# Optimization experiments

Hardware: AMD Instinct MI355X
Metric: run time of the kernel (lower is better)

Reference implementation:

```python
import jax, jax.numpy as jnp
import numpy as np


def setup_inputs() -> dict:
    key = jax.random.key(0)
    kq, kk, kv, ks = jax.random.split(key, 4)
    B, Sq, H, Hkv, D, Dv, Smax = 4, 4, 32, 8, 128, 128, 8192
    Q = jax.random.normal(kq, (B, Sq, H, D), dtype=jnp.float32)
    K = jax.random.normal(kk, (B, Smax, Hkv, D), dtype=jnp.float32)
    V = jax.random.normal(kv, (B, Smax, Hkv, Dv), dtype=jnp.float32)
    # cache lengths well inside [Sq, Smax]
    cache_seqlens = jax.random.randint(ks, (B,), 4096, Smax + 1, dtype=jnp.int32)
    return {"Q": Q, "K": K, "V": V, "cache_seqlens": cache_seqlens}


def reference(Q, K, V, cache_seqlens):
    # Q: [B, Sq, H, D]; K: [B, Smax, Hkv, D]; V: [B, Smax, Hkv, Dv]
    B, Sq, H, D = Q.shape
    Smax, Hkv = K.shape[1], K.shape[2]
    g = H // Hkv  # GQA group size
    scale = 1.0 / (D ** 0.5)

    # Group query heads by their shared KV head to avoid repeating K/V.
    Qg = Q.reshape(B, Sq, Hkv, g, D)
    # scores: [B, Hkv, g, Sq, Smax]
    scores = jnp.einsum("bqhgd,bkhd->bhgqk", Qg, K) * scale

    # Causal-at-cache-end mask: position j valid iff j <= cache_seqlens[b] - Sq + m
    pos = jnp.arange(Smax)
    limit = cache_seqlens[:, None] - Sq + jnp.arange(Sq)[None, :]  # [B, Sq]
    mask = pos[None, None, :] <= limit[:, :, None]                 # [B, Sq, Smax]
    neg_inf = jnp.asarray(-jnp.inf, dtype=scores.dtype)
    scores = jnp.where(mask[:, None, None, :, :], scores, neg_inf)

    attn = jax.nn.softmax(scores, axis=-1)
    out = jnp.einsum("bhgqk,bkhd->bqhgd", attn, V)  # [B, Sq, Hkv, g, Dv]
    return out.reshape(B, Sq, H, V.shape[-1])
```

## Files before the change

kernel.cpp:

```cpp
#include <hip/hip_runtime.h>
#include <hip/hip_bf16.h>
#include <stdint.h>

#define B_    4
#define SQ    4
#define H_    32
#define HKV   8
#define G_    4
#define D_    128
#define SMAX  8192
#define ROWS  16
#define BH    (B_ * HKV)
#define SCALE 0.08838834764831845f
#define MAXSPLITS 64

__device__ __forceinline__ void unpack8(const uint4& u, float* f) {
  f[0] = __uint_as_float(u.x << 16);
  f[1] = __uint_as_float(u.x & 0xffff0000u);
  f[2] = __uint_as_float(u.y << 16);
  f[3] = __uint_as_float(u.y & 0xffff0000u);
  f[4] = __uint_as_float(u.z << 16);
  f[5] = __uint_as_float(u.z & 0xffff0000u);
  f[6] = __uint_as_float(u.w << 16);
  f[7] = __uint_as_float(u.w & 0xffff0000u);
}

__global__ __launch_bounds__(256)
void fa4_sniff(const uint32_t* __restrict__ Kw, int* __restrict__ flag) {
  __shared__ int s_cnt;
  const int t = threadIdx.x;
  if (t == 0) s_cnt = 0;
  __syncthreads();
  int local = 0;
#pragma unroll
  for (int i = 0; i < 4; ++i) {
    const uint32_t w = Kw[t * 4 + i];
    const uint32_t e = (w >> 7) & 0xFFu;
    local += (e >= 100u && e <= 150u) ? 1 : 0;
  }
  atomicAdd(&s_cnt, local);
  __syncthreads();
  if (t == 0) flag[0] = (s_cnt > 700) ? 1 : 0;
}

template<bool BF16>
__device__ __forceinline__ void partial_body(
    const void* __restrict__ Q, const void* __restrict__ K,
    const void* __restrict__ V, const int* __restrict__ lens,
    int splits, int chunk,
    float* __restrict__ Lout, float* __restrict__ acc_out) {
  constexpr int KB  = BF16 ? 16 : 8;
  constexpr int NR  = BF16 ? 1 : 2;
  constexpr int ESZ = BF16 ? 2 : 4;

  const int split = blockIdx.x;
  const int bh    = blockIdx.y;
  const int b     = bh >> 3;
  const int hkv   = bh & 7;
  const int t     = threadIdx.x;
  const int r     = t >> 4;
  const int c     = t & 15;
  const int m     = r >> 2;
  const int gq    = r & 3;
  const int h     = hkv * G_ + gq;

  int len = lens[b];
  if (len > SMAX) len = SMAX;
  if (len < 0)    len = 0;

  const int j0   = split * chunk;
  const int jend = min(j0 + chunk, len);
  const int lim  = len - SQ + m;
  const int vend = min(jend, lim + 1);

  const int sidx = (bh * splits + split) * ROWS + r;
  float* ap = acc_out + (size_t)sidx * D_ + c * 8;

  if (j0 >= vend) {
    if (c == 0) Lout[sidx] = 0.0f;
    const float4 z = make_float4(0.f, 0.f, 0.f, 0.f);
    *(float4*)(ap)     = z;
    *(float4*)(ap + 4) = z;
    return;
  }

  float qf[8];
  {
    const char* qp = (const char*)Q +
        ((size_t)(((b * SQ + m) * H_ + h) * D_) + c * 8) * ESZ;
    if constexpr (BF16) {
      unpack8(*(const uint4*)qp, qf);
    } else {
      const float4 a0 = ((const float4*)qp)[0];
      const float4 a1 = ((const float4*)qp)[1];
      qf[0]=a0.x; qf[1]=a0.y; qf[2]=a0.z; qf[3]=a0.w;
      qf[4]=a1.x; qf[5]=a1.y; qf[6]=a1.z; qf[7]=a1.w;
    }
#pragma unroll
    for (int i = 0; i < 8; ++i) qf[i] *= SCALE;
  }

  const size_t kv0 = ((size_t)b * SMAX * HKV + hkv) * D_ + c * 8;
  const char*  kbase = (const char*)K + kv0 * ESZ;
  const char*  vbase = (const char*)V + kv0 * ESZ;
  constexpr size_t KSTRB = (size_t)HKV * D_ * ESZ;

  float l_run  = 0.0f;
  float acc[8] = {0.f,0.f,0.f,0.f,0.f,0.f,0.f,0.f};

  int j = j0;
  for (; j + KB <= vend; j += KB) {
    uint4 kraw[KB][NR], vraw[KB][NR];
#pragma unroll
    for (int kb = 0; kb < KB; ++kb) {
      const char* kp = kbase + (size_t)(j + kb) * KSTRB;
      const char* vp = vbase + (size_t)(j + kb) * KSTRB;
#pragma unroll
      for (int q = 0; q < NR; ++q) {
        kraw[kb][q] = ((const uint4*)kp)[q];
        vraw[kb][q] = ((const uint4*)vp)[q];
      }
    }
    __builtin_amdgcn_sched_barrier(0);
    float lsum = 0.0f;
#pragma unroll
    for (int kb = 0; kb < KB; ++kb) {
      float kf[8], vf[8];
      if constexpr (BF16) {
        unpack8(kraw[kb][0], kf);
        unpack8(vraw[kb][0], vf);
      } else {
        const float* kk = (const float*)&kraw[kb][0];
        const float* vv = (const float*)&vraw[kb][0];
#pragma unroll
        for (int i = 0; i < 8; ++i) { kf[i] = kk[i]; vf[i] = vv[i]; }
      }
      float p = qf[0] * kf[0];
#pragma unroll
      for (int i = 1; i < 8; ++i) p = fmaf(qf[i], kf[i], p);
      p += __shfl_xor(p, 1, 16);
      p += __shfl_xor(p, 2, 16);
      p += __shfl_xor(p, 4, 16);
      p += __shfl_xor(p, 8, 16);
      const float pw = __expf(p);
      lsum += pw;
#pragma unroll
      for (int i = 0; i < 8; ++i) acc[i] = fmaf(pw, vf[i], acc[i]);
    }
    l_run += lsum;
  }

  if (j < vend) {
    const int jmaxv = vend - 1;
    uint4 kraw[KB][NR], vraw[KB][NR];
#pragma unroll
    for (int kb = 0; kb < KB; ++kb) {
      const int jj = min(j + kb, jmaxv);
      const char* kp = kbase + (size_t)jj * KSTRB;
      const char* vp = vbase + (size_t)jj * KSTRB;
#pragma unroll
      for (int q = 0; q < NR; ++q) {
        kraw[kb][q] = ((const uint4*)kp)[q];
        vraw[kb][q] = ((const uint4*)vp)[q];
      }
    }
    __builtin_amdgcn_sched_barrier(0);
    float lsum = 0.0f;
#pragma unroll
    for (int kb = 0; kb < KB; ++kb) {
      float kf[8], vf[8];
      if constexpr (BF16) {
        unpack8(kraw[kb][0], kf);
        unpack8(vraw[kb][0], vf);
      } else {
        const float* kk = (const float*)&kraw[kb][0];
        const float* vv = (const float*)&vraw[kb][0];
#pragma unroll
        for (int i = 0; i < 8; ++i) { kf[i] = kk[i]; vf[i] = vv[i]; }
      }
      float p = qf[0] * kf[0];
#pragma unroll
      for (int i = 1; i < 8; ++i) p = fmaf(qf[i], kf[i], p);
      p += __shfl_xor(p, 1, 16);
      p += __shfl_xor(p, 2, 16);
      p += __shfl_xor(p, 4, 16);
      p += __shfl_xor(p, 8, 16);
      const float pw = (j + kb <= jmaxv) ? __expf(p) : 0.0f;
      lsum += pw;
#pragma unroll
      for (int i = 0; i < 8; ++i) acc[i] = fmaf(pw, vf[i], acc[i]);
    }
    l_run += lsum;
  }

  if (c == 0) Lout[sidx] = l_run;
  *(float4*)(ap)     = make_float4(acc[0], acc[1], acc[2], acc[3]);
  *(float4*)(ap + 4) = make_float4(acc[4], acc[5], acc[6], acc[7]);
}

__global__
__attribute__((amdgpu_flat_work_group_size(256, 256)))
__attribute__((amdgpu_waves_per_eu(2, 2)))
void fa4_partial(const void* __restrict__ Q, const void* __restrict__ K,
                 const void* __restrict__ V, const int* __restrict__ lens,
                 const int* __restrict__ flag, int splits, int chunk,
                 float* __restrict__ Lout, float* __restrict__ acc_out) {
  if (flag[0] == 1) partial_body<true >(Q, K, V, lens, splits, chunk, Lout, acc_out);
  else              partial_body<false>(Q, K, V, lens, splits, chunk, Lout, acc_out);
}

__global__ __launch_bounds__(256)
void fa4_reduce(const float* __restrict__ Lin,
                const float* __restrict__ acc_in,
                const int* __restrict__ flag, int splits,
                void* __restrict__ out) {
  const int bh  = blockIdx.x;
  const int b   = bh >> 3;
  const int hkv = bh & 7;
  const int t   = threadIdx.x;
  const int r   = t >> 4;
  const int c   = t & 15;
  const int m   = r >> 2;
  const int gq  = r & 3;
  const int h   = hkv * G_ + gq;

  float L = 0.0f;
  float o[8] = {0.f,0.f,0.f,0.f,0.f,0.f,0.f,0.f};
#pragma unroll 4
  for (int s = 0; s < splits; ++s) {
    const size_t row = (size_t)(bh * splits + s) * ROWS + r;
    L += Lin[row];
    const float4* ap = (const float4*)(acc_in + row * D_ + c * 8);
    const float4 a0 = ap[0];
    const float4 a1 = ap[1];
    o[0] += a0.x; o[1] += a0.y; o[2] += a0.z; o[3] += a0.w;
    o[4] += a1.x; o[5] += a1.y; o[6] += a1.z; o[7] += a1.w;
  }
  const float inv = (L > 0.0f) ? (1.0f / L) : 0.0f;
  const size_t oo = ((size_t)(b * SQ + m) * H_ + h) * D_ + c * 8;
  if (flag[0] == 1) {
    unsigned short us[8];
#pragma unroll
    for (int i = 0; i < 8; ++i) {
      const __hip_bfloat16 hb = __float2bfloat16(o[i] * inv);
      __builtin_memcpy(&us[i], &hb, 2);
    }
    uint4 pk;
    pk.x = (uint32_t)us[0] | ((uint32_t)us[1] << 16);
    pk.y = (uint32_t)us[2] | ((uint32_t)us[3] << 16);
    pk.z = (uint32_t)us[4] | ((uint32_t)us[5] << 16);
    pk.w = (uint32_t)us[6] | ((uint32_t)us[7] << 16);
    *(uint4*)((__hip_bfloat16*)out + oo) = pk;
  } else {
    float* op = (float*)out + oo;
    *(float4*)(op)     = make_float4(o[0]*inv, o[1]*inv, o[2]*inv, o[3]*inv);
    *(float4*)(op + 4) = make_float4(o[4]*inv, o[5]*inv, o[6]*inv, o[7]*inv);
  }
}

extern "C" void kernel_launch(void* const* d_in, const int* in_sizes, int n_in,
                              void* d_out, int out_size, void* d_ws, size_t ws_size,
                              hipStream_t stream) {
  const void* Q   = d_in[0];
  const void* K   = d_in[1];
  const void* V   = d_in[2];
  const int* lens = (const int*)d_in[3];

  const size_t per_split = (size_t)BH * ROWS * sizeof(float)
                         + (size_t)BH * ROWS * D_ * sizeof(float);
  int S = 1;
  if (ws_size > 256 + per_split)
    S = (int)((ws_size - 256) / per_split);
  if (S < 1) S = 1;
  if (S > MAXSPLITS) S = MAXSPLITS;
  const int chunk = (SMAX + S - 1) / S;

  int*   flag = (int*)d_ws;
  float* Lbuf = (float*)((char*)d_ws + 256);
  float* acc  = (float*)((char*)d_ws + 256 + (size_t)S * BH * ROWS * sizeof(float));

  fa4_sniff<<<1, 256, 0, stream>>>((const uint32_t*)K, flag);

  dim3 g1(S, BH);
  fa4_partial<<<g1, 256, 0, stream>>>(Q, K, V, lens, flag, S, chunk, Lbuf, acc);
  fa4_reduce<<<BH, 256, 0, stream>>>(Lbuf, acc, flag, S, d_out);
}
```

Baseline: 399.6 us.

## Add MFMA bf16 split-K decode attention path with LDS staging

Replaces the scalar bf16 partial-attention body with a matrix-core path. K and V tiles of 64 keys are staged into LDS with direct global-to-LDS loads and a swizzled K layout. QK^T and PV are computed with 16x16x32 bf16 MFMA; V is fed through transposing LDS reads, and probabilities are split into hi/lo bf16 parts to keep accuracy. Per-wave partial results are reduced through LDS. The fp32 path stays scalar but now shares a kernel that allocates about 33KB of LDS, which may lower its occupancy; MAXSPLITS is also halved.

```diff
diff --git a/kernel.cpp b/kernel.cpp
--- a/kernel.cpp
+++ b/kernel.cpp
@@ -12,7 +12,16 @@
 #define ROWS  16
 #define BH    (B_ * HKV)
 #define SCALE 0.08838834764831845f
-#define MAXSPLITS 64
+#define C2    0.12751743f
+#define MAXSPLITS 32
+#define KSTRB 2048
+#define LDS_K 0
+#define LDS_V 16384
+
+typedef short bf16x8 __attribute__((ext_vector_type(8)));
+typedef float f32x4  __attribute__((ext_vector_type(4)));
+typedef unsigned int u32x2 __attribute__((ext_vector_type(2)));
+typedef unsigned int u32x4 __attribute__((ext_vector_type(4)));
 
 __device__ __forceinline__ void unpack8(const uint4& u, float* f) {
   f[0] = __uint_as_float(u.x << 16);
@@ -25,6 +34,18 @@
   f[7] = __uint_as_float(u.w & 0xffff0000u);
 }
 
+__device__ __forceinline__ uint32_t bf16bits(float x) {
+  __hip_bfloat16 h = __float2bfloat16(x);
+  uint16_t u; __builtin_memcpy(&u, &h, 2);
+  return (uint32_t)u;
+}
+
+__device__ __forceinline__ void g2lds16(const void* g, void* l) {
+  __builtin_amdgcn_global_load_lds(
+      (const __attribute__((address_space(1))) void*)g,
+      (__attribute__((address_space(3))) void*)l, 16, 0, 0);
+}
+
 __global__ __launch_bounds__(256)
 void fa4_sniff(const uint32_t* __restrict__ Kw, int* __restrict__ flag) {
   __shared__ int s_cnt;
@@ -43,15 +64,12 @@
   if (t == 0) flag[0] = (s_cnt > 700) ? 1 : 0;
 }
 
-template<bool BF16>
-__device__ __forceinline__ void partial_body(
+__device__ __forceinline__ void partial_body_f32(
     const void* __restrict__ Q, const void* __restrict__ K,
     const void* __restrict__ V, const int* __restrict__ lens,
     int splits, int chunk,
     float* __restrict__ Lout, float* __restrict__ acc_out) {
-  constexpr int KB  = BF16 ? 16 : 8;
-  constexpr int NR  = BF16 ? 1 : 2;
-  constexpr int ESZ = BF16 ? 2 : 4;
+  constexpr int KB = 8;
 
   const int split = blockIdx.x;
   const int bh    = blockIdx.y;
@@ -86,37 +104,32 @@
 
   float qf[8];
   {
-    const char* qp = (const char*)Q +
-        ((size_t)(((b * SQ + m) * H_ + h) * D_) + c * 8) * ESZ;
-    if constexpr (BF16) {
-      unpack8(*(const uint4*)qp, qf);
-    } else {
-      const float4 a0 = ((const float4*)qp)[0];
-      const float4 a1 = ((const float4*)qp)[1];
-      qf[0]=a0.x; qf[1]=a0.y; qf[2]=a0.z; qf[3]=a0.w;
-      qf[4]=a1.x; qf[5]=a1.y; qf[6]=a1.z; qf[7]=a1.w;
-    }
+    const float4* p = (const float4*)((const float*)Q +
+        (size_t)(((b * SQ + m) * H_ + h) * D_) + c * 8);
+    const float4 a0 = p[0], a1 = p[1];
+    qf[0]=a0.x; qf[1]=a0.y; qf[2]=a0.z; qf[3]=a0.w;
+    qf[4]=a1.x; qf[5]=a1.y; qf[6]=a1.z; qf[7]=a1.w;
 #pragma unroll
     for (int i = 0; i < 8; ++i) qf[i] *= SCALE;
   }
 
   const size_t kv0 = ((size_t)b * SMAX * HKV + hkv) * D_ + c * 8;
-  const char*  kbase = (const char*)K + kv0 * ESZ;
-  const char*  vbase = (const char*)V + kv0 * ESZ;
-  constexpr size_t KSTRB = (size_t)HKV * D_ * ESZ;
+  const char*  kbase = (const char*)K + kv0 * 4;
+  const char*  vbase = (const char*)V + kv0 * 4;
+  const size_t kstrb = (size_t)HKV * D_ * 4;
 
   float l_run  = 0.0f;
   float acc[8] = {0.f,0.f,0.f,0.f,0.f,0.f,0.f,0.f};
 
   int j = j0;
   for (; j + KB <= vend; j += KB) {
-    uint4 kraw[KB][NR], vraw[KB][NR];
+    uint4 kraw[KB][2], vraw[KB][2];
 #pragma unroll
     for (int kb = 0; kb < KB; ++kb) {
-      const char* kp = kbase + (size_t)(j + kb) * KSTRB;
-      const char* vp = vbase + (size_t)(j + kb) * KSTRB;
-#pragma unroll
-      for (int q = 0; q < NR; ++q) {
+      const char* kp = kbase + (size_t)(j + kb) * kstrb;
+      const char* vp = vbase + (size_t)(j + kb) * kstrb;
+#pragma unroll
+      for (int q = 0; q < 2; ++q) {
         kraw[kb][q] = ((const uint4*)kp)[q];
         vraw[kb][q] = ((const uint4*)vp)[q];
       }
@@ -125,19 +138,11 @@
     float lsum = 0.0f;
 #pragma unroll
     for (int kb = 0; kb < KB; ++kb) {
-      float kf[8], vf[8];
-      if constexpr (BF16) {
-        unpack8(kraw[kb][0], kf);
-        unpack8(vraw[kb][0], vf);
-      } else {
-        const float* kk = (const float*)&kraw[kb][0];
-        const float* vv = (const float*)&vraw[kb][0];
-#pragma unroll
-        for (int i = 0; i < 8; ++i) { kf[i] = kk[i]; vf[i] = vv[i]; }
-      }
-      float p = qf[0] * kf[0];
-#pragma unroll
-      for (int i = 1; i < 8; ++i) p = fmaf(qf[i], kf[i], p);
+      const float* kk = (const float*)&kraw[kb][0];
+      const float* vv = (const float*)&vraw[kb][0];
+      float p = qf[0] * kk[0];
+#pragma unroll
+      for (int i = 1; i < 8; ++i) p = fmaf(qf[i], kk[i], p);
       p += __shfl_xor(p, 1, 16);
       p += __shfl_xor(p, 2, 16);
       p += __shfl_xor(p, 4, 16);
@@ -145,21 +150,21 @@
       const float pw = __expf(p);
       lsum += pw;
 #pragma unroll
-      for (int i = 0; i < 8; ++i) acc[i] = fmaf(pw, vf[i], acc[i]);
+      for (int i = 0; i < 8; ++i) acc[i] = fmaf(pw, vv[i], acc[i]);
     }
     l_run += lsum;
   }
 
   if (j < vend) {
     const int jmaxv = vend - 1;
-    uint4 kraw[KB][NR], vraw[KB][NR];
+    uint4 kraw[KB][2], vraw[KB][2];
 #pragma unroll
     for (int kb = 0; kb < KB; ++kb) {
       const int jj = min(j + kb, jmaxv);
-      const char* kp = kbase + (size_t)jj * KSTRB;
-      const char* vp = vbase + (size_t)jj * KSTRB;
-#pragma unroll
-      for (int q = 0; q < NR; ++q) {
+      const char* kp = kbase + (size_t)jj * kstrb;
+      const char* vp = vbase + (size_t)jj * kstrb;
+#pragma unroll
+      for (int q = 0; q < 2; ++q) {
         kraw[kb][q] = ((const uint4*)kp)[q];
         vraw[kb][q] = ((const uint4*)vp)[q];
       }
@@ -168,19 +173,11 @@
     float lsum = 0.0f;
 #pragma unroll
     for (int kb = 0; kb < KB; ++kb) {
-      float kf[8], vf[8];
-      if constexpr (BF16) {
-        unpack8(kraw[kb][0], kf);
-        unpack8(vraw[kb][0], vf);
-      } else {
-        const float* kk = (const float*)&kraw[kb][0];
-        const float* vv = (const float*)&vraw[kb][0];
-#pragma unroll
-        for (int i = 0; i < 8; ++i) { kf[i] = kk[i]; vf[i] = vv[i]; }
-      }
-      float p = qf[0] * kf[0];
-#pragma unroll
-      for (int i = 1; i < 8; ++i) p = fmaf(qf[i], kf[i], p);
+      const float* kk = (const float*)&kraw[kb][0];
+      const float* vv = (const float*)&vraw[kb][0];
+      float p = qf[0] * kk[0];
+#pragma unroll
+      for (int i = 1; i < 8; ++i) p = fmaf(qf[i], kk[i], p);
       p += __shfl_xor(p, 1, 16);
       p += __shfl_xor(p, 2, 16);
       p += __shfl_xor(p, 4, 16);
@@ -188,7 +185,7 @@
       const float pw = (j + kb <= jmaxv) ? __expf(p) : 0.0f;
       lsum += pw;
 #pragma unroll
-      for (int i = 0; i < 8; ++i) acc[i] = fmaf(pw, vf[i], acc[i]);
+      for (int i = 0; i < 8; ++i) acc[i] = fmaf(pw, vv[i], acc[i]);
     }
     l_run += lsum;
   }
@@ -198,15 +195,172 @@
   *(float4*)(ap + 4) = make_float4(acc[4], acc[5], acc[6], acc[7]);
 }
 
-__global__
-__attribute__((amdgpu_flat_work_group_size(256, 256)))
-__attribute__((amdgpu_waves_per_eu(2, 2)))
+__device__ __forceinline__ void mfma_body(
+    const void* __restrict__ Q, const void* __restrict__ K,
+    const void* __restrict__ V, const int* __restrict__ lens,
+    int splits, int chunk,
+    float* __restrict__ Lout, float* __restrict__ acc_out, char* smem) {
+  const int split = blockIdx.x;
+  const int bh    = blockIdx.y;
+  const int b     = bh >> 3;
+  const int hkv   = bh & 7;
+  const int t     = threadIdx.x;
+  const int w     = t >> 6;
+  const int lane  = t & 63;
+  const int lg    = lane >> 4;
+  const int lc    = lane & 15;
+
+  int len = lens[b];
+  if (len > SMAX) len = SMAX;
+  if (len < 0)    len = 0;
+
+  const int j0    = split * chunk;
+  const int jend  = min(j0 + chunk, len);
+  const int sbase = (bh * splits + split) * ROWS;
+
+  if (j0 >= jend) {
+    const int row = t >> 4, c = t & 15;
+    float* ap = acc_out + (size_t)(sbase + row) * D_ + c * 8;
+    const float4 z = make_float4(0.f, 0.f, 0.f, 0.f);
+    *(float4*)ap = z; *(float4*)(ap + 4) = z;
+    if (t < 16) Lout[sbase + t] = 0.f;
+    return;
+  }
+
+  const int rho = lc, qm = rho >> 2, gq = rho & 3;
+  const char* Qb = (const char*)Q;
+  const size_t qbyte =
+      (((size_t)(b * SQ + qm) * H_ + hkv * G_ + gq) * D_ + (size_t)lg * 8) * 2;
+  bf16x8 qf[4];
+#pragma unroll
+  for (int kc = 0; kc < 4; ++kc)
+    qf[kc] = *(const bf16x8*)(Qb + qbyte + kc * 64);
+
+  const int vmax = min(jend - 1, len - SQ + qm);
+
+  const size_t kvbyte0 = ((size_t)b * SMAX * HKV + hkv) * D_ * 2;
+  const char* Kb = (const char*)K + kvbyte0;
+  const char* Vb = (const char*)V + kvbyte0;
+
+  f32x4 acc[8];
+#pragma unroll
+  for (int i = 0; i < 8; ++i) acc[i] = (f32x4)0.f;
+  float Lacc = 0.f;
+
+  for (int tb = j0; tb < jend; tb += 64) {
+#pragma unroll
+    for (int q = 0; q < 4; ++q) {
+      const int idx  = (w * 4 + q) * 64 + lane;
+      const int key  = idx >> 4;
+      const int slot = idx & 15;
+      const int j    = min(tb + key, len - 1);
+      g2lds16(Kb + (size_t)j * KSTRB + (size_t)((slot ^ (key & 15)) << 4),
+              smem + LDS_K + (w * 4 + q) * 1024);
+    }
+#pragma unroll
+    for (int q = 0; q < 4; ++q) {
+      const int cidx  = (w * 4 + q) * 64 + lane;
+      const int dvh   = cidx & 1;
+      const int key16 = (cidx >> 1) & 15;
+      const int t8    = (cidx >> 5) & 7;
+      const int sub2  = cidx >> 8;
+      const int j     = min(tb + sub2 * 16 + key16, len - 1);
+      g2lds16(Vb + (size_t)j * KSTRB + (size_t)(t8 * 32 + dvh * 16),
+              smem + LDS_V + (w * 4 + q) * 1024);
+    }
+    __syncthreads();
+
+    f32x4 s = (f32x4)0.f;
+    const char* krow = smem + LDS_K + (w * 16 + lc) * 256;
+#pragma unroll
+    for (int kc = 0; kc < 4; ++kc) {
+      bf16x8 kf = *(const bf16x8*)(krow + (((kc * 4 + lg) ^ lc) << 4));
+      s = __builtin_amdgcn_mfma_f32_16x16x32_bf16(kf, qf[kc], s, 0, 0, 0);
+    }
+
+    const int key0 = tb + w * 16 + lg * 4;
+    float pw[4];
+#pragma unroll
+    for (int j4 = 0; j4 < 4; ++j4)
+      pw[j4] = (key0 + j4 <= vmax) ? exp2f(s[j4] * C2) : 0.f;
+    Lacc += (pw[0] + pw[1]) + (pw[2] + pw[3]);
+
+    uint32_t hb[4], lb[4];
+#pragma unroll
+    for (int j4 = 0; j4 < 4; ++j4) {
+      hb[j4] = bf16bits(pw[j4]);
+      const float hf = __uint_as_float(hb[j4] << 16);
+      lb[j4] = bf16bits(pw[j4] - hf);
+    }
+    u32x4 pa;
+    pa.x = hb[0] | (hb[1] << 16);
+    pa.y = hb[2] | (hb[3] << 16);
+    pa.z = lb[0] | (lb[1] << 16);
+    pa.w = lb[2] | (lb[3] << 16);
+    const bf16x8 pfrag = __builtin_bit_cast(bf16x8, pa);
+
+    typedef __attribute__((address_space(3))) const char* ldsp;
+    u32x2 tr[8];
+    ldsp vb3 = (ldsp)(smem + LDS_V + w * 4096 + lg * 128 + lc * 2);
+    asm volatile("ds_read_b64_tr_b16 %0, %1 offset:0"    : "=v"(tr[0]) : "v"(vb3));
+    asm volatile("ds_read_b64_tr_b16 %0, %1 offset:512"  : "=v"(tr[1]) : "v"(vb3));
+    asm volatile("ds_read_b64_tr_b16 %0, %1 offset:1024" : "=v"(tr[2]) : "v"(vb3));
+    asm volatile("ds_read_b64_tr_b16 %0, %1 offset:1536" : "=v"(tr[3]) : "v"(vb3));
+    asm volatile("ds_read_b64_tr_b16 %0, %1 offset:2048" : "=v"(tr[4]) : "v"(vb3));
+    asm volatile("ds_read_b64_tr_b16 %0, %1 offset:2560" : "=v"(tr[5]) : "v"(vb3));
+    asm volatile("ds_read_b64_tr_b16 %0, %1 offset:3072" : "=v"(tr[6]) : "v"(vb3));
+    asm volatile("ds_read_b64_tr_b16 %0, %1 offset:3584" : "=v"(tr[7]) : "v"(vb3));
+    asm volatile("s_waitcnt lgkmcnt(0)" ::: "memory");
+    __builtin_amdgcn_sched_barrier(0);
+
+#pragma unroll
+    for (int t8 = 0; t8 < 8; ++t8) {
+      u32x4 vv;
+      vv.x = tr[t8].x; vv.y = tr[t8].y; vv.z = tr[t8].x; vv.w = tr[t8].y;
+      const bf16x8 vf = __builtin_bit_cast(bf16x8, vv);
+      acc[t8] = __builtin_amdgcn_mfma_f32_16x16x32_bf16(pfrag, vf, acc[t8], 0, 0, 0);
+    }
+    __syncthreads();
+  }
+
+  float* accbuf = (float*)smem;
+  float* Lb     = (float*)(smem + 32768);
+#pragma unroll
+  for (int t8 = 0; t8 < 8; ++t8)
+#pragma unroll
+    for (int j4 = 0; j4 < 4; ++j4)
+      accbuf[w * 2048 + (lg * 4 + j4) * 128 + t8 * 16 + lc] = acc[t8][j4];
+  float Ls = Lacc;
+  Ls += __shfl_xor(Ls, 16);
+  Ls += __shfl_xor(Ls, 32);
+  if (lane < 16) Lb[w * 16 + lane] = Ls;
+  __syncthreads();
+
+  const int row = t >> 4, c = t & 15;
+  float o[8] = {0.f,0.f,0.f,0.f,0.f,0.f,0.f,0.f};
+#pragma unroll
+  for (int ww = 0; ww < 4; ++ww) {
+    const float4* p = (const float4*)(accbuf + ww * 2048 + row * 128 + c * 8);
+    const float4 a0 = p[0], a1 = p[1];
+    o[0]+=a0.x; o[1]+=a0.y; o[2]+=a0.z; o[3]+=a0.w;
+    o[4]+=a1.x; o[5]+=a1.y; o[6]+=a1.z; o[7]+=a1.w;
+  }
+  float* ap = acc_out + (size_t)(sbase + row) * D_ + c * 8;
+  *(float4*)ap       = make_float4(o[0], o[1], o[2], o[3]);
+  *(float4*)(ap + 4) = make_float4(o[4], o[5], o[6], o[7]);
+  if (t < 16) Lout[sbase + t] = Lb[t] + Lb[16 + t] + Lb[32 + t] + Lb[48 + t];
+}
+
+__global__ __launch_bounds__(256, 2)
 void fa4_partial(const void* __restrict__ Q, const void* __restrict__ K,
                  const void* __restrict__ V, const int* __restrict__ lens,
                  const int* __restrict__ flag, int splits, int chunk,
                  float* __restrict__ Lout, float* __restrict__ acc_out) {
-  if (flag[0] == 1) partial_body<true >(Q, K, V, lens, splits, chunk, Lout, acc_out);
-  else              partial_body<false>(Q, K, V, lens, splits, chunk, Lout, acc_out);
+  __shared__ char smem[33792];
+  if (flag[0] == 1)
+    mfma_body(Q, K, V, lens, splits, chunk, Lout, acc_out, smem);
+  else
+    partial_body_f32(Q, K, V, lens, splits, chunk, Lout, acc_out);
 }
 
 __global__ __launch_bounds__(256)
@@ -242,8 +396,8 @@
     unsigned short us[8];
 #pragma unroll
     for (int i = 0; i < 8; ++i) {
-      const __hip_bfloat16 hb = __float2bfloat16(o[i] * inv);
-      __builtin_memcpy(&us[i], &hb, 2);
+      const __hip_bfloat16 hb2 = __float2bfloat16(o[i] * inv);
+      __builtin_memcpy(&us[i], &hb2, 2);
     }
     uint4 pk;
     pk.x = (uint32_t)us[0] | ((uint32_t)us[1] << 16);
```

Result: no change. 392.9 us (-1.7%).
